# Kernel optimization log

Hardware: AMD Instinct MI355X
Metric: run time of the kernel (lower is better)

Reference implementation:

```python
import jax, jax.numpy as jnp
import numpy as np

INPUT_DIM, QK_DIM, V_DIM = 1024, 512, 512

def setup_inputs() -> dict:
    key = jax.random.key(0)
    ks = jax.random.split(key, 7)
    B, S = 4, 2048
    scale = 1.0 / np.sqrt(INPUT_DIM)
    return {
        "x": jax.random.normal(ks[0], (B, S, INPUT_DIM), dtype=jnp.float32),
        "Wq": jax.random.normal(ks[1], (INPUT_DIM, QK_DIM), dtype=jnp.float32) * scale,
        "bq": jax.random.normal(ks[2], (QK_DIM,), dtype=jnp.float32) * 0.01,
        "Wk": jax.random.normal(ks[3], (INPUT_DIM, QK_DIM), dtype=jnp.float32) * scale,
        "bk": jax.random.normal(ks[4], (QK_DIM,), dtype=jnp.float32) * 0.01,
        "Wv": jax.random.normal(ks[5], (INPUT_DIM, V_DIM), dtype=jnp.float32) * scale,
        "bv": jax.random.normal(ks[6], (V_DIM,), dtype=jnp.float32) * 0.01,
    }

def reference(x, Wq, bq, Wk, bk, Wv, bv):
    # q,k: (B,S,Dqk), v: (B,S,Dv)
    q = jnp.einsum("bsi,id->bsd", x, Wq) + bq
    k = jnp.einsum("bsi,id->bsd", x, Wk) + bk
    v = jnp.einsum("bsi,id->bsd", x, Wv) + bv
    scale = 1.0 / jnp.sqrt(jnp.asarray(q.shape[-1], q.dtype))
    scores = jnp.einsum("bqd,bkd->bqk", q, k) * scale  # (B,S,S)
    attn = jax.nn.softmax(scores, axis=-1)
    return jnp.einsum("bqk,bkd->bqd", attn, v)
```

## Files before the change

### kernel.cpp

```cpp
#include <hip/hip_runtime.h>

typedef __attribute__((ext_vector_type(8))) short short8;
typedef __attribute__((ext_vector_type(4))) float f32x4;

#define S_    2048
#define DI    1024
#define DQK   512
#define DV    512
#define NTOK  8192
#define CSTR  136
#define CS2   264

#define GLL(gp, lp) __builtin_amdgcn_global_load_lds( \
    (const __attribute__((address_space(1))) unsigned int*)(gp), \
    (__attribute__((address_space(3))) unsigned int*)(lp), 16, 0, 0)

static __device__ __forceinline__ unsigned short f2bf(float f) {
  unsigned int u = __float_as_uint(f);
  u += 0x7fffu + ((u >> 16) & 1u);
  return (unsigned short)(u >> 16);
}

__global__ void prep_kernel(const float* __restrict__ x, unsigned short* __restrict__ xb,
                            const float* __restrict__ W0, const float* __restrict__ W1,
                            const float* __restrict__ W2,
                            unsigned short* __restrict__ T0, unsigned short* __restrict__ T1,
                            unsigned short* __restrict__ T2,
                            float* __restrict__ rowsum) {
  __shared__ float tile[32][33];
  int bid = blockIdx.x;
  if (bid < 4096) {
    int idx = (bid * 256 + threadIdx.x) * 8;
    const float4* p = (const float4*)(x + idx);
    float4 f0 = p[0], f1 = p[1];
    uint4 o;
    o.x = (unsigned)f2bf(f0.x) | ((unsigned)f2bf(f0.y) << 16);
    o.y = (unsigned)f2bf(f0.z) | ((unsigned)f2bf(f0.w) << 16);
    o.z = (unsigned)f2bf(f1.x) | ((unsigned)f2bf(f1.y) << 16);
    o.w = (unsigned)f2bf(f1.z) | ((unsigned)f2bf(f1.w) << 16);
    *(uint4*)(xb + idx) = o;
    return;
  }
  int b2 = bid - 4096;
  int mat = b2 >> 9;
  int rem = b2 & 511;
  if (mat == 0 && rem < 32) rowsum[rem * 256 + threadIdx.x] = 0.f;
  const float* W = (mat == 0) ? W0 : (mat == 1) ? W1 : W2;
  unsigned short* T = (mat == 0) ? T0 : (mat == 1) ? T1 : T2;
  int n0 = (rem & 15) * 32, k0 = (rem >> 4) * 32;
  int c = threadIdx.x & 31, r0 = threadIdx.x >> 5;
  for (int i = 0; i < 4; ++i) {
    int kk = r0 + i * 8;
    tile[kk][c] = W[(k0 + kk) * DQK + n0 + c];
  }
  __syncthreads();
  for (int i = 0; i < 4; ++i) {
    int nn = r0 + i * 8;
    T[(n0 + nn) * DI + k0 + c] = f2bf(tile[c][nn]);
  }
}

__device__ __forceinline__ void gemm_core_dbuf(
    const unsigned short* __restrict__ A, const unsigned short* __restrict__ B,
    int lda, int ldb, int K, int m0, int n0,
    unsigned short (*As)[128 * 32], unsigned short (*Bs)[128 * 32],
    f32x4 (&acc)[4][4]) {
  int tid = threadIdx.x, lane = tid & 63, wv = tid >> 6;
  int quad = lane >> 4, l16 = lane & 15;
  int wm = wv >> 1, wn = wv & 1;
  int srow = tid >> 2;
  int sc = (tid & 3) ^ (srow & 3);
  const unsigned short* gA0 = A + (size_t)(m0 + srow) * lda + sc * 8;
  const unsigned short* gA1 = A + (size_t)(m0 + 64 + srow) * lda + sc * 8;
  const unsigned short* gB0 = B + (size_t)(n0 + srow) * ldb + sc * 8;
  const unsigned short* gB1 = B + (size_t)(n0 + 64 + srow) * ldb + sc * 8;
  int d0 = wv * 512;
  int d1 = 2048 + wv * 512;
#pragma unroll
  for (int i = 0; i < 4; ++i)
#pragma unroll
    for (int j = 0; j < 4; ++j) acc[i][j] = (f32x4){0.f, 0.f, 0.f, 0.f};

  auto stage = [&](int buf, int k0) {
    GLL(gA0 + k0, &As[buf][d0]);
    GLL(gA1 + k0, &As[buf][d1]);
    GLL(gB0 + k0, &Bs[buf][d0]);
    GLL(gB1 + k0, &Bs[buf][d1]);
  };

  int pc = (quad ^ (l16 & 3)) * 8;
  int nk = K >> 5;
  stage(0, 0);
  for (int kt = 0; kt < nk; ++kt) {
    int cur = kt & 1;
    __syncthreads();
    if (kt + 1 < nk) stage(cur ^ 1, (kt + 1) * 32);
    short8 af[4], bf[4];
#pragma unroll
    for (int t = 0; t < 4; ++t) {
      af[t] = *(const short8*)(&As[cur][(wm * 64 + t * 16 + l16) * 32 + pc]);
      bf[t] = *(const short8*)(&Bs[cur][(wn * 64 + t * 16 + l16) * 32 + pc]);
    }
#pragma unroll
    for (int tm = 0; tm < 4; ++tm)
#pragma unroll
      for (int tn = 0; tn < 4; ++tn)
        acc[tm][tn] = __builtin_amdgcn_mfma_f32_16x16x32_bf16(af[tm], bf[tn], acc[tm][tn], 0, 0, 0);
  }
}

__global__ __launch_bounds__(256, 3) void qkv_dma_kernel(
    const unsigned short* __restrict__ xb,
    const unsigned short* __restrict__ wqt, const unsigned short* __restrict__ wkt,
    const unsigned short* __restrict__ wvt,
    const float* __restrict__ bq, const float* __restrict__ bk, const float* __restrict__ bv,
    unsigned short* __restrict__ qo, unsigned short* __restrict__ ko,
    unsigned short* __restrict__ vto) {
  __shared__ unsigned short smem[128 * CSTR];
  unsigned short (*As)[4096] = (unsigned short (*)[4096])smem;
  unsigned short (*Bs)[4096] = (unsigned short (*)[4096])(smem + 8192);
  int bidx = blockIdx.x;
  int xcd = bidx & 7;
  int local = bidx >> 3;
  int mlocal = local & 7;
  int col12 = local >> 3;
  int mat = col12 >> 2;
  int m0 = (xcd * 8 + mlocal) * 128;
  int n0 = (col12 & 3) * 128;
  const unsigned short* wt = (mat == 0) ? wqt : (mat == 1) ? wkt : wvt;
  const float* bias = (mat == 0) ? bq : (mat == 1) ? bk : bv;
  float oscale = (mat == 0) ? 0.04419417382415922f : 1.0f;
  f32x4 acc[4][4];
  gemm_core_dbuf(xb, wt, DI, DI, DI, m0, n0, As, Bs, acc);

  int tid = threadIdx.x, lane = tid & 63, wv = tid >> 6;
  int quad = lane >> 4, l16 = lane & 15;
  int wm = wv >> 1, wn = wv & 1;
  bool transp = (mat == 2);
  __syncthreads();
#pragma unroll
  for (int tn = 0; tn < 4; ++tn) {
    int cl = wn * 64 + tn * 16 + l16;
    float bc = bias[n0 + cl];
#pragma unroll
    for (int tm = 0; tm < 4; ++tm) {
      int rl = wm * 64 + tm * 16 + quad * 4;
      f32x4 a = acc[tm][tn];
      unsigned short v0 = f2bf((a.x + bc) * oscale);
      unsigned short v1 = f2bf((a.y + bc) * oscale);
      unsigned short v2 = f2bf((a.z + bc) * oscale);
      unsigned short v3 = f2bf((a.w + bc) * oscale);
      if (!transp) {
        smem[(rl + 0) * CSTR + cl] = v0;
        smem[(rl + 1) * CSTR + cl] = v1;
        smem[(rl + 2) * CSTR + cl] = v2;
        smem[(rl + 3) * CSTR + cl] = v3;
      } else {
        smem[cl * CSTR + rl + 0] = v0;
        smem[cl * CSTR + rl + 1] = v1;
        smem[cl * CSTR + rl + 2] = v2;
        smem[cl * CSTR + rl + 3] = v3;
      }
    }
  }
  __syncthreads();
  int r = tid >> 1, half = (tid & 1) * 64;
  if (!transp) {
    unsigned short* outp = (mat == 0) ? qo : ko;
    unsigned short* gp = outp + (size_t)(m0 + r) * DQK + n0 + half;
#pragma unroll
    for (int j = 0; j < 8; ++j)
      *(uint4*)(gp + j * 8) = *(const uint4*)(smem + r * CSTR + half + j * 8);
  } else {
    unsigned short* gp = vto + (size_t)(n0 + r) * NTOK + m0 + half;
#pragma unroll
    for (int j = 0; j < 8; ++j)
      *(uint4*)(gp + j * 8) = *(const uint4*)(smem + r * CSTR + half + j * 8);
  }
}

__global__ __launch_bounds__(256, 2) void s_exp_kernel(
    const unsigned short* __restrict__ q, const unsigned short* __restrict__ k,
    unsigned short* __restrict__ sp, float* __restrict__ rowsum) {
  __shared__ unsigned short smem[24576];
  int bidx = blockIdx.x;
  int xcd = bidx & 7, b = xcd >> 1;
  int sub = ((bidx >> 3) << 1) | (xcd & 1);
  int m0 = (sub >> 3) * 128, n0 = (sub & 7) * 256;
  int tid = threadIdx.x, lane = tid & 63, wv = tid >> 6;
  int quad = lane >> 4, l16 = lane & 15;
  int wm = wv >> 1, wn = wv & 1;
  const unsigned short* qb = q + (size_t)b * S_ * DQK;
  const unsigned short* kb = k + (size_t)b * S_ * DQK;

  int srow = tid >> 2;
  int sc = (tid & 3) ^ (srow & 3);
  const unsigned short* gA0 = qb + (size_t)(m0 + srow) * DQK + sc * 8;
  const unsigned short* gA1 = qb + (size_t)(m0 + 64 + srow) * DQK + sc * 8;
  const unsigned short* gB0 = kb + (size_t)(n0 + srow) * DQK + sc * 8;
  const unsigned short* gB1 = kb + (size_t)(n0 + 64 + srow) * DQK + sc * 8;
  const unsigned short* gB2 = kb + (size_t)(n0 + 128 + srow) * DQK + sc * 8;
  const unsigned short* gB3 = kb + (size_t)(n0 + 192 + srow) * DQK + sc * 8;
  int dA0 = (wv * 16) * 32, dA1 = (64 + wv * 16) * 32;

  f32x4 acc[4][8];
#pragma unroll
  for (int i = 0; i < 4; ++i)
#pragma unroll
    for (int j = 0; j < 8; ++j) acc[i][j] = (f32x4){0.f, 0.f, 0.f, 0.f};

  auto stage = [&](int buf, int k0) {
    unsigned short* base = smem + buf * 12288;
    GLL(gA0 + k0, base + dA0);
    GLL(gA1 + k0, base + dA1);
    unsigned short* bb = base + 4096;
    GLL(gB0 + k0, bb + dA0);
    GLL(gB1 + k0, bb + dA1);
    GLL(gB2 + k0, bb + (128 + wv * 16) * 32);
    GLL(gB3 + k0, bb + (192 + wv * 16) * 32);
  };

  int pc = (quad ^ (l16 & 3)) * 8;
  stage(0, 0);
  for (int kt = 0; kt < 16; ++kt) {
    int cur = kt & 1;
    __syncthreads();
    if (kt + 1 < 16) stage(cur ^ 1, (kt + 1) * 32);
    const unsigned short* base = smem + cur * 12288;
    short8 af[4], bf[8];
#pragma unroll
    for (int t = 0; t < 4; ++t)
      af[t] = *(const short8*)(base + (wm * 64 + t * 16 + l16) * 32 + pc);
#pragma unroll
    for (int t = 0; t < 8; ++t)
      bf[t] = *(const short8*)(base + 4096 + (wn * 128 + t * 16 + l16) * 32 + pc);
#pragma unroll
    for (int tm = 0; tm < 4; ++tm)
#pragma unroll
      for (int tn = 0; tn < 8; ++tn)
        acc[tm][tn] = __builtin_amdgcn_mfma_f32_16x16x32_bf16(af[tm], bf[tn], acc[tm][tn], 0, 0, 0);
  }

#pragma unroll
  for (int tm = 0; tm < 4; ++tm) {
    int rl = wm * 64 + tm * 16 + quad * 4;
    float rs[4] = {0.f, 0.f, 0.f, 0.f};
#pragma unroll
    for (int tn = 0; tn < 8; ++tn) {
      f32x4 a = acc[tm][tn];
      a.x = __expf(a.x); a.y = __expf(a.y); a.z = __expf(a.z); a.w = __expf(a.w);
      acc[tm][tn] = a;
      rs[0] += a.x; rs[1] += a.y; rs[2] += a.z; rs[3] += a.w;
    }
    for (int off = 1; off < 16; off <<= 1)
#pragma unroll
      for (int r = 0; r < 4; ++r) rs[r] += __shfl_xor(rs[r], off);
    if (l16 == 0)
#pragma unroll
      for (int r = 0; r < 4; ++r) atomicAdd(rowsum + b * S_ + m0 + rl + r, rs[r]);
  }

  unsigned short* spb = sp + (size_t)b * S_ * S_;
  int cr = tid >> 2, cq = (tid & 3) * 64;
#pragma unroll
  for (int h = 0; h < 2; ++h) {
    __syncthreads();
    if (wm == h) {
#pragma unroll
      for (int tm = 0; tm < 4; ++tm) {
        int rl = tm * 16 + quad * 4;
#pragma unroll
        for (int tn = 0; tn < 8; ++tn) {
          int cl = wn * 128 + tn * 16 + l16;
          f32x4 a = acc[tm][tn];
          smem[(rl + 0) * CS2 + cl] = f2bf(a.x);
          smem[(rl + 1) * CS2 + cl] = f2bf(a.y);
          smem[(rl + 2) * CS2 + cl] = f2bf(a.z);
          smem[(rl + 3) * CS2 + cl] = f2bf(a.w);
        }
      }
    }
    __syncthreads();
    unsigned short* gp = spb + (size_t)(m0 + h * 64 + cr) * S_ + n0 + cq;
#pragma unroll
    for (int j = 0; j < 8; ++j)
      *(uint4*)(gp + j * 8) = *(const uint4*)(smem + cr * CS2 + cq + j * 8);
  }
}

__global__ __launch_bounds__(256, 4) void pv_kernel(
    const unsigned short* __restrict__ sp, const unsigned short* __restrict__ vt,
    const float* __restrict__ rowsum, float* __restrict__ out) {
  __shared__ unsigned short smem[16384];
  unsigned short (*As)[4096] = (unsigned short (*)[4096])smem;
  unsigned short (*Bs)[4096] = (unsigned short (*)[4096])(smem + 8192);
  int bidx = blockIdx.x;
  int xcd = bidx & 7, b = xcd >> 1;
  int sub = ((bidx >> 3) << 1) | (xcd & 1);
  int m0 = (sub >> 3) * 64, n0 = (sub & 7) * 64;
  int tid = threadIdx.x, lane = tid & 63, wv = tid >> 6;
  int quad = lane >> 4, l16 = lane & 15;
  int wm = wv >> 1, wn = wv & 1;
  const unsigned short* A = sp + (size_t)b * S_ * S_;
  const unsigned short* B = vt + (size_t)b * S_;

  int srow = tid >> 3;
  int schunk = (tid & 7) ^ (srow & 7);
  const unsigned short* gA0 = A + (size_t)(m0 + srow) * S_ + schunk * 8;
  const unsigned short* gA1 = A + (size_t)(m0 + 32 + srow) * S_ + schunk * 8;
  const unsigned short* gB0 = B + (size_t)(n0 + srow) * NTOK + schunk * 8;
  const unsigned short* gB1 = B + (size_t)(n0 + 32 + srow) * NTOK + schunk * 8;
  int ldsw0 = (wv * 8) * 64;
  int ldsw1 = (32 + wv * 8) * 64;

  f32x4 acc[2][2];
#pragma unroll
  for (int i = 0; i < 2; ++i)
#pragma unroll
    for (int j = 0; j < 2; ++j) acc[i][j] = (f32x4){0.f, 0.f, 0.f, 0.f};

  auto stage = [&](int buf, int k0) {
    GLL(gA0 + k0, &As[buf][ldsw0]);
    GLL(gA1 + k0, &As[buf][ldsw1]);
    GLL(gB0 + k0, &Bs[buf][ldsw0]);
    GLL(gB1 + k0, &Bs[buf][ldsw1]);
  };

  stage(0, 0);
  for (int kt = 0; kt < 32; ++kt) {
    int cur = kt & 1;
    __syncthreads();
    if (kt + 1 < 32) stage(cur ^ 1, (kt + 1) * 64);
#pragma unroll
    for (int ks = 0; ks < 2; ++ks) {
      int pc = ((ks * 4 + quad) ^ (l16 & 7)) * 8;
      short8 af[2], bf[2];
#pragma unroll
      for (int t = 0; t < 2; ++t) {
        af[t] = *(const short8*)(&As[cur][(wm * 32 + t * 16 + l16) * 64 + pc]);
        bf[t] = *(const short8*)(&Bs[cur][(wn * 32 + t * 16 + l16) * 64 + pc]);
      }
#pragma unroll
      for (int tm = 0; tm < 2; ++tm)
#pragma unroll
        for (int tn = 0; tn < 2; ++tn)
          acc[tm][tn] = __builtin_amdgcn_mfma_f32_16x16x32_bf16(af[tm], bf[tn], acc[tm][tn], 0, 0, 0);
    }
  }

  float* ct = (float*)smem;
  __syncthreads();
#pragma unroll
  for (int tm = 0; tm < 2; ++tm) {
    int rl = wm * 32 + tm * 16 + quad * 4;
    float inv[4];
#pragma unroll
    for (int i = 0; i < 4; ++i) inv[i] = 1.0f / rowsum[b * S_ + m0 + rl + i];
#pragma unroll
    for (int tn = 0; tn < 2; ++tn) {
      int cl = wn * 32 + tn * 16 + l16;
      f32x4 a = acc[tm][tn];
      ct[(rl + 0) * 68 + cl] = a.x * inv[0];
      ct[(rl + 1) * 68 + cl] = a.y * inv[1];
      ct[(rl + 2) * 68 + cl] = a.z * inv[2];
      ct[(rl + 3) * 68 + cl] = a.w * inv[3];
    }
  }
  __syncthreads();
  int r = tid >> 2, qc = (tid & 3) * 16;
  float* ob = out + (size_t)b * S_ * DV + (size_t)(m0 + r) * DV + n0 + qc;
#pragma unroll
  for (int j = 0; j < 4; ++j)
    *(uint4*)(ob + j * 4) = *(const uint4*)(ct + r * 68 + qc + j * 4);
}

extern "C" void kernel_launch(void* const* d_in, const int* in_sizes, int n_in,
                              void* d_out, int out_size, void* d_ws, size_t ws_size,
                              hipStream_t stream) {
  const float* x  = (const float*)d_in[0];
  const float* Wq = (const float*)d_in[1];
  const float* bq = (const float*)d_in[2];
  const float* Wk = (const float*)d_in[3];
  const float* bk = (const float*)d_in[4];
  const float* Wv = (const float*)d_in[5];
  const float* bv = (const float*)d_in[6];
  float* out = (float*)d_out;

  char* ws = (char*)d_ws;
  unsigned short* xb  = (unsigned short*)(ws);
  unsigned short* wqt = (unsigned short*)(ws + 16777216);
  unsigned short* wkt = (unsigned short*)(ws + 16777216 + 1048576);
  unsigned short* wvt = (unsigned short*)(ws + 16777216 + 2097152);
  unsigned short* qo  = (unsigned short*)(ws + 19922944);
  unsigned short* ko  = (unsigned short*)(ws + 19922944 + 8388608);
  unsigned short* vto = (unsigned short*)(ws + 19922944 + 16777216);
  unsigned short* sp  = (unsigned short*)(ws + 45088768);
  float* rowsum       = (float*)(ws + 45088768 + 33554432);

  prep_kernel<<<5632, 256, 0, stream>>>(x, xb, Wq, Wk, Wv, wqt, wkt, wvt, rowsum);
  qkv_dma_kernel<<<768, 256, 0, stream>>>(xb, wqt, wkt, wvt, bq, bk, bv, qo, ko, vto);
  s_exp_kernel<<<512, 256, 0, stream>>>(qo, ko, sp, rowsum);
  pv_kernel<<<1024, 256, 0, stream>>>(sp, vto, rowsum, out);
}
```

Measured before the change: 186.1 us.

## Enlarge PV kernel tile to 128x128 with 512 threads and K-step 32

The P·V kernel moves from 64x64 output tiles on 256-thread blocks to 128x128 tiles on 512-thread blocks with 8 waves. The K step drops to 32 and the LDS swizzle changes to match. The epilogue now writes through shared memory in four row slabs. Larger tiles are meant to halve re-reads of the large bf16 score matrix and the V tile per output element. In exchange the grid shrinks to 256 blocks, which is about one per CU, so fewer blocks are resident and there are twice as many barriers per K.

New measurement: 192.7 us. 1.04x slower.

```diff
diff --git a/kernel.cpp b/kernel.cpp
--- a/kernel.cpp
+++ b/kernel.cpp
@@ -288,90 +288,90 @@
   }
 }
 
-__global__ __launch_bounds__(256, 4) void pv_kernel(
+__global__ __launch_bounds__(512, 1) void pv_kernel(
     const unsigned short* __restrict__ sp, const unsigned short* __restrict__ vt,
     const float* __restrict__ rowsum, float* __restrict__ out) {
   __shared__ unsigned short smem[16384];
-  unsigned short (*As)[4096] = (unsigned short (*)[4096])smem;
-  unsigned short (*Bs)[4096] = (unsigned short (*)[4096])(smem + 8192);
   int bidx = blockIdx.x;
   int xcd = bidx & 7, b = xcd >> 1;
   int sub = ((bidx >> 3) << 1) | (xcd & 1);
-  int m0 = (sub >> 3) * 64, n0 = (sub & 7) * 64;
+  int m0 = (sub >> 2) * 128, n0 = (sub & 3) * 128;
   int tid = threadIdx.x, lane = tid & 63, wv = tid >> 6;
   int quad = lane >> 4, l16 = lane & 15;
   int wm = wv >> 1, wn = wv & 1;
   const unsigned short* A = sp + (size_t)b * S_ * S_;
   const unsigned short* B = vt + (size_t)b * S_;
 
-  int srow = tid >> 3;
-  int schunk = (tid & 7) ^ (srow & 7);
-  const unsigned short* gA0 = A + (size_t)(m0 + srow) * S_ + schunk * 8;
-  const unsigned short* gA1 = A + (size_t)(m0 + 32 + srow) * S_ + schunk * 8;
-  const unsigned short* gB0 = B + (size_t)(n0 + srow) * NTOK + schunk * 8;
-  const unsigned short* gB1 = B + (size_t)(n0 + 32 + srow) * NTOK + schunk * 8;
-  int ldsw0 = (wv * 8) * 64;
-  int ldsw1 = (32 + wv * 8) * 64;
-
-  f32x4 acc[2][2];
+  int srow = tid >> 2;
+  int sc = (tid & 3) ^ (srow & 3);
+  const unsigned short* gA = A + (size_t)(m0 + srow) * S_ + sc * 8;
+  const unsigned short* gB = B + (size_t)(n0 + srow) * NTOK + sc * 8;
+  int d = (wv * 16) * 32;
+
+  f32x4 acc[2][4];
 #pragma unroll
   for (int i = 0; i < 2; ++i)
 #pragma unroll
-    for (int j = 0; j < 2; ++j) acc[i][j] = (f32x4){0.f, 0.f, 0.f, 0.f};
+    for (int j = 0; j < 4; ++j) acc[i][j] = (f32x4){0.f, 0.f, 0.f, 0.f};
 
   auto stage = [&](int buf, int k0) {
-    GLL(gA0 + k0, &As[buf][ldsw0]);
-    GLL(gA1 + k0, &As[buf][ldsw1]);
-    GLL(gB0 + k0, &Bs[buf][ldsw0]);
-    GLL(gB1 + k0, &Bs[buf][ldsw1]);
+    GLL(gA + k0, smem + buf * 4096 + d);
+    GLL(gB + k0, smem + 8192 + buf * 4096 + d);
   };
 
+  int pc = (quad ^ (l16 & 3)) * 8;
   stage(0, 0);
-  for (int kt = 0; kt < 32; ++kt) {
+  for (int kt = 0; kt < 64; ++kt) {
     int cur = kt & 1;
     __syncthreads();
-    if (kt + 1 < 32) stage(cur ^ 1, (kt + 1) * 64);
-#pragma unroll
-    for (int ks = 0; ks < 2; ++ks) {
-      int pc = ((ks * 4 + quad) ^ (l16 & 7)) * 8;
-      short8 af[2], bf[2];
-#pragma unroll
-      for (int t = 0; t < 2; ++t) {
-        af[t] = *(const short8*)(&As[cur][(wm * 32 + t * 16 + l16) * 64 + pc]);
-        bf[t] = *(const short8*)(&Bs[cur][(wn * 32 + t * 16 + l16) * 64 + pc]);
+    if (kt + 1 < 64) stage(cur ^ 1, (kt + 1) * 32);
+    const unsigned short* ab = smem + cur * 4096;
+    const unsigned short* bb = smem + 8192 + cur * 4096;
+    short8 af[2], bf[4];
+#pragma unroll
+    for (int t = 0; t < 2; ++t)
+      af[t] = *(const short8*)(ab + (wm * 32 + t * 16 + l16) * 32 + pc);
+#pragma unroll
+    for (int t = 0; t < 4; ++t)
+      bf[t] = *(const short8*)(bb + (wn * 64 + t * 16 + l16) * 32 + pc);
+#pragma unroll
+    for (int tm = 0; tm < 2; ++tm)
+#pragma unroll
+      for (int tn = 0; tn < 4; ++tn)
+        acc[tm][tn] = __builtin_amdgcn_mfma_f32_16x16x32_bf16(af[tm], bf[tn], acc[tm][tn], 0, 0, 0);
+  }
+
+  float inv[2][4];
+#pragma unroll
+  for (int tm = 0; tm < 2; ++tm)
+#pragma unroll
+    for (int i = 0; i < 4; ++i)
+      inv[tm][i] = 1.0f / rowsum[b * S_ + m0 + wm * 32 + tm * 16 + quad * 4 + i];
+  float* ct = (float*)smem;
+  int cr = tid >> 4, cq = (tid & 15) * 8;
+#pragma unroll
+  for (int h = 0; h < 4; ++h) {
+    __syncthreads();
+    if (wm == h) {
+#pragma unroll
+      for (int tm = 0; tm < 2; ++tm) {
+        int rl = tm * 16 + quad * 4;
+#pragma unroll
+        for (int tn = 0; tn < 4; ++tn) {
+          int cl = wn * 64 + tn * 16 + l16;
+          f32x4 a = acc[tm][tn];
+          ct[(rl + 0) * 132 + cl] = a.x * inv[tm][0];
+          ct[(rl + 1) * 132 + cl] = a.y * inv[tm][1];
+          ct[(rl + 2) * 132 + cl] = a.z * inv[tm][2];
+          ct[(rl + 3) * 132 + cl] = a.w * inv[tm][3];
+        }
       }
-#pragma unroll
-      for (int tm = 0; tm < 2; ++tm)
-#pragma unroll
-        for (int tn = 0; tn < 2; ++tn)
-          acc[tm][tn] = __builtin_amdgcn_mfma_f32_16x16x32_bf16(af[tm], bf[tn], acc[tm][tn], 0, 0, 0);
     }
-  }
-
-  float* ct = (float*)smem;
-  __syncthreads();
-#pragma unroll
-  for (int tm = 0; tm < 2; ++tm) {
-    int rl = wm * 32 + tm * 16 + quad * 4;
-    float inv[4];
-#pragma unroll
-    for (int i = 0; i < 4; ++i) inv[i] = 1.0f / rowsum[b * S_ + m0 + rl + i];
-#pragma unroll
-    for (int tn = 0; tn < 2; ++tn) {
-      int cl = wn * 32 + tn * 16 + l16;
-      f32x4 a = acc[tm][tn];
-      ct[(rl + 0) * 68 + cl] = a.x * inv[0];
-      ct[(rl + 1) * 68 + cl] = a.y * inv[1];
-      ct[(rl + 2) * 68 + cl] = a.z * inv[2];
-      ct[(rl + 3) * 68 + cl] = a.w * inv[3];
-    }
-  }
-  __syncthreads();
-  int r = tid >> 2, qc = (tid & 3) * 16;
-  float* ob = out + (size_t)b * S_ * DV + (size_t)(m0 + r) * DV + n0 + qc;
-#pragma unroll
-  for (int j = 0; j < 4; ++j)
-    *(uint4*)(ob + j * 4) = *(const uint4*)(ct + r * 68 + qc + j * 4);
+    __syncthreads();
+    float* ob = out + (size_t)b * S_ * DV + (size_t)(m0 + h * 32 + cr) * DV + n0 + cq;
+    *(uint4*)(ob + 0) = *(const uint4*)(ct + cr * 132 + cq + 0);
+    *(uint4*)(ob + 4) = *(const uint4*)(ct + cr * 132 + cq + 4);
+  }
 }
 
 extern "C" void kernel_launch(void* const* d_in, const int* in_sizes, int n_in,
@@ -400,5 +400,5 @@
   prep_kernel<<<5632, 256, 0, stream>>>(x, xb, Wq, Wk, Wv, wqt, wkt, wvt, rowsum);
   qkv_dma_kernel<<<768, 256, 0, stream>>>(xb, wqt, wkt, wvt, bq, bk, bv, qo, ko, vto);
   s_exp_kernel<<<512, 256, 0, stream>>>(qo, ko, sp, rowsum);
-  pv_kernel<<<1024, 256, 0, stream>>>(sp, vto, rowsum, out);
-}
+  pv_kernel<<<256, 512, 0, stream>>>(sp, vto, rowsum, out);
+}
```
